# Performance work log

Hardware: AMD Instinct MI355X
Metric: run time of the kernel (lower is better)

The kernel has to match this reference:

```python
import jax, jax.numpy as jnp
import numpy as np

T, B, I, H, O = 512, 128, 512, 512, 12

def setup_inputs() -> dict:
    key = jax.random.key(0)
    ks = jax.random.split(key, 17)
    def w(k, shape):
        # xavier-normal-ish init
        std = float(np.sqrt(2.0 / (shape[0] + shape[-1])))
        return jax.random.normal(k, shape, dtype=jnp.float32) * std
    return {
        "x": jax.random.normal(ks[0], (T, B, I), dtype=jnp.float32),
        "w0": w(ks[1], (O, H)), "wz": w(ks[2], (O, H)), "wr": w(ks[3], (O, H)),
        "ws": w(ks[4], (I, H)),
        "wa": w(ks[5], (H, H)), "ua": w(ks[6], (I, H)), "va": w(ks[7], (H, 1)),
        "u0": w(ks[8], (H, H)), "uz": w(ks[9], (H, H)), "ur": w(ks[10], (H, H)),
        "c0": w(ks[11], (I, H)), "cz": w(ks[12], (I, H)), "cr": w(ks[13], (I, H)),
        "fc_w": w(ks[14], (H, O)),
        "fc_b": jnp.zeros((O,), dtype=jnp.float32),
        "max_labels": 16,
    }

def reference(x, w0, wz, wr, ws, wa, ua, va, u0, uz, ur, c0, cz, cr, fc_w, fc_b, max_labels):
    # x: [T, B, I] encoder states; decode max_labels steps of a Bahdanau-attention GRU.
    s0 = jnp.tanh(x[0] @ ws)              # [B, H]
    out0 = s0 @ fc_w + fc_b               # [B, O]
    U = jnp.einsum('tbi,ih->tbh', x, ua)  # precomputed encoder projection
    va_v = va[:, 0]                       # [H]

    def step(carry, _):
        s, out = carry                                          # [B,H], [B,O]
        e = jnp.einsum('tbh,h->tb', jnp.tanh(s @ wa + U), va_v)  # [T,B] additive scores
        a = jax.nn.softmax(e, axis=0)                           # attention over T
        c = jnp.einsum('tb,tbi->bi', a, x)                      # [B,I] context
        r = jax.nn.sigmoid(out @ wr + s @ ur + c @ cr)
        z = jax.nn.sigmoid(out @ wz + s @ uz + c @ cz)
        sh = jnp.tanh(out @ w0 + (r * s) @ u0 + c @ c0)
        s_new = (1.0 - z) * s + z * sh
        out_new = s_new @ fc_w + fc_b
        return (s_new, out_new), out_new

    _, outs = jax.lax.scan(step, (s0, out0), None, length=max_labels - 1)
    all_outs = jnp.concatenate([out0[None], outs], axis=0)  # [L, B, O]
    return jnp.transpose(all_outs, (1, 0, 2))               # [B, L, O]
```

## Files before the change

kernel.cpp:

```cpp
#include <hip/hip_runtime.h>

#define NSTEP 16

typedef __attribute__((ext_vector_type(8))) short s16x8;
typedef __attribute__((ext_vector_type(4))) float f32x4;
typedef __attribute__((ext_vector_type(2))) float f32x2;

__device__ __forceinline__ float bf2f(unsigned short u){
  union { unsigned int i; float f; } v; v.i = ((unsigned int)u) << 16; return v.f;
}
__device__ __forceinline__ unsigned short f2bf(float f){
  union { float f; unsigned int i; } v; v.f = f;
  unsigned int r = v.i + 0x7fffu + ((v.i >> 16) & 1u);
  return (unsigned short)(r >> 16);
}
__device__ __forceinline__ float fast_rcp(float x){ return __builtin_amdgcn_rcpf(x); }
__device__ __forceinline__ float fast_tanh(float x){
  float e = __expf(2.0f * x);
  return 1.0f - 2.0f * fast_rcp(e + 1.0f);
}
__device__ __forceinline__ float fast_sigmoid(float x){
  return fast_rcp(1.0f + __expf(-x));
}
__device__ __forceinline__ void gload16(const void* g, void* l){
  __builtin_amdgcn_global_load_lds((const __attribute__((address_space(1))) void*)g,
                                   (__attribute__((address_space(3))) void*)l, 16, 0, 0);
}
__device__ __forceinline__ float wave_sum(float v){
#pragma unroll
  for (int off = 32; off; off >>= 1) v += __shfl_xor(v, off, 64);
  return v;
}
__device__ __forceinline__ void fp8x8_dec(uint2 w, float* u){
  f32x2 d0 = __builtin_amdgcn_cvt_pk_f32_fp8(w.x, false);
  f32x2 d1 = __builtin_amdgcn_cvt_pk_f32_fp8(w.x, true);
  f32x2 d2 = __builtin_amdgcn_cvt_pk_f32_fp8(w.y, false);
  f32x2 d3 = __builtin_amdgcn_cvt_pk_f32_fp8(w.y, true);
  u[0] = d0[0]; u[1] = d0[1]; u[2] = d1[0]; u[3] = d1[1];
  u[4] = d2[0]; u[5] = d2[1]; u[6] = d3[0]; u[7] = d3[1];
}
__device__ __forceinline__ s16x8 f32x8_to_bf8(float4 a, float4 b){
  s16x8 t8;
  t8[0] = (short)f2bf(a.x); t8[1] = (short)f2bf(a.y);
  t8[2] = (short)f2bf(a.z); t8[3] = (short)f2bf(a.w);
  t8[4] = (short)f2bf(b.x); t8[5] = (short)f2bf(b.y);
  t8[6] = (short)f2bf(b.z); t8[7] = (short)f2bf(b.w);
  return t8;
}
__device__ __forceinline__ uint2 f32x8_to_fp8(float4 a, float4 b){
  unsigned int lo, hi;
  lo = __builtin_amdgcn_cvt_pk_fp8_f32(a.x, a.y, 0, false);
  lo = __builtin_amdgcn_cvt_pk_fp8_f32(a.z, a.w, lo, true);
  hi = __builtin_amdgcn_cvt_pk_fp8_f32(b.x, b.y, 0, false);
  hi = __builtin_amdgcn_cvt_pk_fp8_f32(b.z, b.w, hi, true);
  uint2 w; w.x = lo; w.y = hi;
  return w;
}
__device__ __forceinline__ unsigned char f2fp8(float f){
  return (unsigned char)(__builtin_amdgcn_cvt_pk_fp8_f32(f, f, 0, false) & 0xff);
}

struct GemmLDS { unsigned short A[128 * 64]; unsigned short B[128 * 64]; };

__global__ __launch_bounds__(512) void uxc_k(
    const float* __restrict__ x, const unsigned short* __restrict__ Bt,
    unsigned char* __restrict__ U8, unsigned char* __restrict__ x8){
  __shared__ GemmLDS lds;
  const int tid = threadIdx.x;
  const int lane = tid & 63, wid = tid >> 6;
  const int wr = wid >> 2, wc = wid & 3;
  const int mt = blockIdx.y, nt = blockIdx.x;
  f32x4 acc[4][2];
#pragma unroll
  for (int m = 0; m < 4; ++m)
#pragma unroll
    for (int n = 0; n < 2; ++n) acc[m][n] = (f32x4)0.0f;

  for (int kt = 0; kt < 512; kt += 64){
    __syncthreads();
    {
      bool emit = (kt >> 7) == nt;
#pragma unroll
      for (int i = 0; i < 2; ++i){
        int s = i * 512 + tid;
        int row = s >> 3, c8 = s & 7;
        int sc = c8 ^ (row & 7);
        size_t goff = (size_t)(mt * 128 + row) * 512 + kt + sc * 8;
        const float* ap = x + goff;
        float4 a0 = *(const float4*)ap, a1 = *(const float4*)(ap + 4);
        *(s16x8*)&lds.A[s * 8] = f32x8_to_bf8(a0, a1);
        if (emit) *(uint2*)(x8 + goff) = f32x8_to_fp8(a0, a1);
      }
#pragma unroll
      for (int p = 0; p < 2; ++p){
        int s = p * 512 + tid;
        int br = s >> 3, bkc = (s & 7) ^ (br & 7);
        gload16(Bt + (size_t)(nt * 128 + br) * 512 + kt + bkc * 8, &lds.B[s * 8]);
      }
    }
    __syncthreads();
#pragma unroll
    for (int ks = 0; ks < 2; ++ks){
      int kc_l = (lane >> 4) + ks * 4;
      s16x8 av[4], bv[2];
#pragma unroll
      for (int m = 0; m < 4; ++m){
        int r = wr * 64 + m * 16 + (lane & 15);
        av[m] = *(const s16x8*)&lds.A[r * 64 + ((kc_l ^ (r & 7)) << 3)];
      }
#pragma unroll
      for (int n = 0; n < 2; ++n){
        int c = wc * 32 + n * 16 + (lane & 15);
        bv[n] = *(const s16x8*)&lds.B[c * 64 + ((kc_l ^ (c & 7)) << 3)];
      }
#pragma unroll
      for (int m = 0; m < 4; ++m)
#pragma unroll
        for (int n = 0; n < 2; ++n)
          acc[m][n] = __builtin_amdgcn_mfma_f32_16x16x32_bf16(av[m], bv[n], acc[m][n], 0, 0, 0);
    }
  }
#pragma unroll
  for (int m = 0; m < 4; ++m)
#pragma unroll
    for (int n = 0; n < 2; ++n){
      int r_base = mt * 128 + wr * 64 + m * 16 + ((lane >> 4) << 2);
      int col = nt * 128 + wc * 32 + n * 16 + (lane & 15);
#pragma unroll
      for (int q = 0; q < 4; ++q)
        U8[(size_t)(r_base + q) * 512 + col] = f2fp8(acc[m][n][q]);
    }
}

struct FLDS { unsigned short A[64 * 256]; unsigned short B[64 * 256]; };

template<int EPI, bool AF32>
__device__ __forceinline__ void fgemm_body(int mt, int nt,
    const unsigned short* __restrict__ A, const float* __restrict__ Af,
    const unsigned short* __restrict__ Bt,
    unsigned short* __restrict__ ob0, float* __restrict__ o0,
    const float* __restrict__ e0, const float* __restrict__ e1,
    const float* __restrict__ e2, FLDS& lds){
  const int tid = threadIdx.x;
  const int lane = tid & 63, wid = tid >> 6;
  const int wr = wid >> 1, wc = wid & 1;
  f32x4 acc[2];
  acc[0] = (f32x4)0.0f; acc[1] = (f32x4)0.0f;

  for (int kt = 0; kt < 512; kt += 256){
    if (kt) __syncthreads();
#pragma unroll
    for (int i = 0; i < 4; ++i){
      int s = i * 512 + tid;
      int row = s >> 5, c = s & 31;
      int sc = (c & 24) | ((c & 7) ^ (row & 7));
      if constexpr (AF32){
        const float* ap = Af + (size_t)(mt * 64 + row) * 512 + kt + sc * 8;
        float4 a0 = *(const float4*)ap, a1 = *(const float4*)(ap + 4);
        *(s16x8*)&lds.A[s * 8] = f32x8_to_bf8(a0, a1);
      } else {
        gload16(A + (size_t)(mt * 64 + row) * 512 + kt + sc * 8, &lds.A[s * 8]);
      }
      gload16(Bt + (size_t)(nt * 64 + row) * 512 + kt + sc * 8, &lds.B[s * 8]);
    }
    __syncthreads();
#pragma unroll
    for (int kk = 0; kk < 8; ++kk){
      int kch = kk * 4 + (lane >> 4);
      int ar = wr * 16 + (lane & 15);
      int asw = (kch & 24) | ((kch & 7) ^ (ar & 7));
      s16x8 av = *(const s16x8*)&lds.A[ar * 256 + asw * 8];
#pragma unroll
      for (int n = 0; n < 2; ++n){
        int br = wc * 32 + n * 16 + (lane & 15);
        int bsw = (kch & 24) | ((kch & 7) ^ (br & 7));
        s16x8 bv = *(const s16x8*)&lds.B[br * 256 + bsw * 8];
        acc[n] = __builtin_amdgcn_mfma_f32_16x16x32_bf16(av, bv, acc[n], 0, 0, 0);
      }
    }
  }

#pragma unroll
  for (int n = 0; n < 2; ++n){
    int r_base = mt * 64 + wr * 16 + ((lane >> 4) << 2);
    int col = nt * 64 + wc * 32 + n * 16 + (lane & 15);
#pragma unroll
    for (int q = 0; q < 4; ++q){
      float v = acc[n][q];
      size_t r_ = (size_t)(r_base + q);
      if constexpr (EPI == 1){
        float t = fast_tanh(v);
        o0[r_ * 512 + col] = t;
        ob0[r_ * 512 + col] = f2bf(t);
      } else if constexpr (EPI == 2){
        o0[r_ * 2048 + col] = v + e0[col];
      } else if constexpr (EPI == 4){
        float v2 = v + e0[r_ * 512 + col];
        float sh = fast_tanh(v2);
        float z  = e1[r_ * 512 + col];
        float so = e2[r_ * 512 + col];
        float sn = (1.0f - z) * so + z * sh;
        o0[r_ * 512 + col] = sn;
        ob0[r_ * 512 + col] = f2bf(sn);
      }
    }
  }
}

template<int EPI, bool AF32>
__global__ __launch_bounds__(512) void fgemm_k(
    const unsigned short* __restrict__ A, const float* __restrict__ Af,
    const unsigned short* __restrict__ Bt,
    unsigned short* __restrict__ ob0, float* __restrict__ o0,
    const float* __restrict__ e0, const float* __restrict__ e1,
    const float* __restrict__ e2){
  __shared__ FLDS lds;
  fgemm_body<EPI, AF32>(blockIdx.y, blockIdx.x, A, Af, Bt, ob0, o0, e0, e1, e2, lds);
}

__global__ __launch_bounds__(512) void ec_k(const unsigned char* __restrict__ U8,
    const unsigned char* __restrict__ x8, const float* __restrict__ pre1,
    const float* __restrict__ va, float* __restrict__ cpart, float* __restrict__ psum){
  __shared__ float cred[8][512];
  __shared__ float pred[8];
  int chunk = blockIdx.x, b = blockIdx.y;
  int tid = threadIdx.x, lane = tid & 63, wid = tid >> 6;
  const float* pp = pre1 + (size_t)b * 2048 + lane * 8;
  float4 p0 = *(const float4*)pp, p1 = *(const float4*)(pp + 4);
  const float* vp = va + lane * 8;
  float4 v0 = *(const float4*)vp, v1 = *(const float4*)(vp + 4);
  float sv[8] = {p0.x, p0.y, p0.z, p0.w, p1.x, p1.y, p1.z, p1.w};
  float vv[8] = {v0.x, v0.y, v0.z, v0.w, v1.x, v1.y, v1.z, v1.w};
  float acc[8] = {0, 0, 0, 0, 0, 0, 0, 0};
  float psum_l = 0.f;
  int t0 = chunk * 256 + wid * 32;
  for (int i = 0; i < 32; ++i){
    int t = t0 + i;
    uint2 w = *(const uint2*)(U8 + ((size_t)t * 128 + b) * 512 + lane * 8);
    float u[8];
    fp8x8_dec(w, u);
    float e = 0.f;
#pragma unroll
    for (int k = 0; k < 8; ++k)
      e += fast_tanh(u[k] + sv[k]) * vv[k];
    e = wave_sum(e);
    float p = __expf(e);
    psum_l += p;
    uint2 wx = *(const uint2*)(x8 + ((size_t)t * 128 + b) * 512 + lane * 8);
    float ux[8];
    fp8x8_dec(wx, ux);
#pragma unroll
    for (int k = 0; k < 8; ++k) acc[k] += p * ux[k];
  }
#pragma unroll
  for (int k = 0; k < 8; ++k) cred[wid][lane * 8 + k] = acc[k];
  if (lane == 0) pred[wid] = psum_l;
  __syncthreads();
  float cs = 0.f;
#pragma unroll
  for (int w = 0; w < 8; ++w) cs += cred[w][tid];
  cpart[((size_t)chunk * 128 + b) * 512 + tid] = cs;
  if (tid == 0){
    float s = 0.f;
#pragma unroll
    for (int w = 0; w < 8; ++w) s += pred[w];
    psum[chunk * 128 + b] = s;
  }
}

__global__ __launch_bounds__(512) void gates_k(
    const float* __restrict__ cpart, const float* __restrict__ psum,
    const unsigned short* __restrict__ P2w, const float* __restrict__ pre1,
    const float* __restrict__ s_prev,
    unsigned short* __restrict__ rsb, float* __restrict__ zbuf, float* __restrict__ cu0){
  __shared__ FLDS lds;
  __shared__ float rden_s[64];
  const int tid = threadIdx.x;
  const int lane = tid & 63, wid = tid >> 6;
  const int wr = wid >> 1, wc = wid & 1;
  const int nt = blockIdx.x, mt = blockIdx.y;
  if (tid < 64){
    float d = psum[mt * 64 + tid] + psum[128 + mt * 64 + tid];
    rden_s[tid] = fast_rcp(d);
  }
  f32x4 acc[2];
  acc[0] = (f32x4)0.0f; acc[1] = (f32x4)0.0f;

  for (int kt = 0; kt < 512; kt += 256){
    __syncthreads();
#pragma unroll
    for (int i = 0; i < 4; ++i){
      int s = i * 512 + tid;
      int row = s >> 5, c = s & 31;
      int sc = (c & 24) | ((c & 7) ^ (row & 7));
      int b = mt * 64 + row;
      const float* cp0 = cpart + (size_t)b * 512 + kt + sc * 8;
      const float* cp1 = cp0 + (size_t)128 * 512;
      float rd = rden_s[row];
      float4 a0 = *(const float4*)cp0, a1 = *(const float4*)(cp0 + 4);
      float4 b0 = *(const float4*)cp1, b1 = *(const float4*)(cp1 + 4);
      s16x8 t8;
      t8[0] = (short)f2bf((a0.x + b0.x) * rd); t8[1] = (short)f2bf((a0.y + b0.y) * rd);
      t8[2] = (short)f2bf((a0.z + b0.z) * rd); t8[3] = (short)f2bf((a0.w + b0.w) * rd);
      t8[4] = (short)f2bf((a1.x + b1.x) * rd); t8[5] = (short)f2bf((a1.y + b1.y) * rd);
      t8[6] = (short)f2bf((a1.z + b1.z) * rd); t8[7] = (short)f2bf((a1.w + b1.w) * rd);
      *(s16x8*)&lds.A[s * 8] = t8;
      gload16(P2w + (size_t)(nt * 64 + row) * 512 + kt + sc * 8, &lds.B[s * 8]);
    }
    __syncthreads();
#pragma unroll
    for (int kk = 0; kk < 8; ++kk){
      int kch = kk * 4 + (lane >> 4);
      int ar = wr * 16 + (lane & 15);
      int asw = (kch & 24) | ((kch & 7) ^ (ar & 7));
      s16x8 av = *(const s16x8*)&lds.A[ar * 256 + asw * 8];
#pragma unroll
      for (int n = 0; n < 2; ++n){
        int br = wc * 32 + n * 16 + (lane & 15);
        int bsw = (kch & 24) | ((kch & 7) ^ (br & 7));
        s16x8 bv = *(const s16x8*)&lds.B[br * 256 + bsw * 8];
        acc[n] = __builtin_amdgcn_mfma_f32_16x16x32_bf16(av, bv, acc[n], 0, 0, 0);
      }
    }
  }

#pragma unroll
  for (int n = 0; n < 2; ++n){
    int r_base = mt * 64 + wr * 16 + ((lane >> 4) << 2);
    int col = nt * 64 + wc * 32 + n * 16 + (lane & 15);
#pragma unroll
    for (int q = 0; q < 4; ++q){
      float v = acc[n][q];
      size_t r_ = (size_t)(r_base + q);
      float v2 = v + pre1[r_ * 2048 + 512 + col];
      if (col < 512){
        float rg = fast_sigmoid(v2);
        rsb[r_ * 512 + col] = f2bf(rg * s_prev[r_ * 512 + col]);
      } else if (col < 1024){
        zbuf[r_ * 512 + (col - 512)] = fast_sigmoid(v2);
      } else {
        cu0[r_ * 512 + (col - 1024)] = v2;
      }
    }
  }
}

__global__ __launch_bounds__(512) void dout_k(const float* __restrict__ s_hist,
    const float* __restrict__ fcwT, const float* __restrict__ fcb,
    float* __restrict__ dout){
  int lane = threadIdx.x & 63, wid = threadIdx.x >> 6;
  int w = blockIdx.x * 8 + wid;
  int step = w >> 7, b = w & 127;
  const float* sp = s_hist + (size_t)w * 512 + lane * 8;
  float4 sa = *(const float4*)sp, sb = *(const float4*)(sp + 4);
#pragma unroll
  for (int o = 0; o < 12; ++o){
    const float* fp = fcwT + (size_t)o * 512 + lane * 8;
    float4 fa = *(const float4*)fp, fb = *(const float4*)(fp + 4);
    float sum = sa.x * fa.x + sa.y * fa.y + sa.z * fa.z + sa.w * fa.w +
                sb.x * fb.x + sb.y * fb.y + sb.z * fb.z + sb.w * fb.w;
    sum = wave_sum(sum);
    if (lane == 0)
      dout[(size_t)b * (NSTEP * 12) + step * 12 + o] = sum + fcb[o];
  }
}

__global__ __launch_bounds__(512) void trans_k(
    const float* __restrict__ ua, const float* __restrict__ wsm,
    const float* __restrict__ u0, const float* __restrict__ wa,
    const float* __restrict__ urm, const float* __restrict__ uz,
    const float* __restrict__ cr, const float* __restrict__ cz,
    const float* __restrict__ c0, const float* __restrict__ wrm,
    const float* __restrict__ wzm, const float* __restrict__ w0m,
    const float* __restrict__ fcw, const float* __restrict__ fcb,
    unsigned short* __restrict__ Pua, unsigned short* __restrict__ Pws,
    unsigned short* __restrict__ P3w, unsigned short* __restrict__ P1w,
    unsigned short* __restrict__ P2w, float* __restrict__ fcwT,
    float* __restrict__ bias_full){
  __shared__ unsigned short tr[64][72];
  int bid = blockIdx.x, tid = threadIdx.x;
  if (bid < 640){
    int mi = bid >> 6, tile = bid & 63;
    int trr = tile >> 3, tcc = tile & 7;
    const float* src = nullptr; const float* W = nullptr; unsigned short* dst;
    switch (mi){
      case 0: src = ua;  dst = Pua;               break;
      case 1: src = wsm; dst = Pws;               break;
      case 2: src = u0;  dst = P3w;               break;
      case 3: src = wa;  dst = P1w;               break;
      case 4: src = urm; dst = P1w + 512 * 512;  W = wrm; break;
      case 5: src = uz;  dst = P1w + 1024 * 512; W = wzm; break;
      case 6: src = nullptr; dst = P1w + 1536 * 512; W = w0m; break;
      case 7: src = cr;  dst = P2w;               break;
      case 8: src = cz;  dst = P2w + 512 * 512;   break;
      default:src = c0;  dst = P2w + 1024 * 512;  break;
    }
    int r = tid >> 3, c8 = (tid & 7) * 8;
    int h = trr * 64 + r;
    float vals[8];
    if (src){
      const float* sp = src + (size_t)h * 512 + tcc * 64 + c8;
      float4 a = *(const float4*)sp, b = *(const float4*)(sp + 4);
      vals[0] = a.x; vals[1] = a.y; vals[2] = a.z; vals[3] = a.w;
      vals[4] = b.x; vals[5] = b.y; vals[6] = b.z; vals[7] = b.w;
    } else {
#pragma unroll
      for (int k = 0; k < 8; ++k) vals[k] = 0.f;
    }
    if (W){
      float fr[12];
#pragma unroll
      for (int o = 0; o < 12; ++o) fr[o] = fcw[h * 12 + o];
#pragma unroll
      for (int jj = 0; jj < 8; ++jj){
        int j = tcc * 64 + c8 + jj;
        float cj = 0.f;
#pragma unroll
        for (int o = 0; o < 12; ++o) cj += fr[o] * W[o * 512 + j];
        vals[jj] += cj;
      }
    }
    unsigned short* lp = &tr[r][c8];
#pragma unroll
    for (int k = 0; k < 8; ++k) lp[k] = f2bf(vals[k]);
    __syncthreads();
    s16x8 o8v;
#pragma unroll
    for (int k = 0; k < 8; ++k) o8v[k] = (short)tr[c8 + k][r];
    *(s16x8*)(dst + (size_t)(tcc * 64 + r) * 512 + trr * 64 + c8) = o8v;
  } else if (bid < 652){
    int gidx = (bid - 640) * 512 + tid;
    int h = gidx / 12, o = gidx - h * 12;
    fcwT[(size_t)o * 512 + h] = fcw[h * 12 + o];
  } else {
#pragma unroll
    for (int p = 0; p < 4; ++p){
      int col = p * 512 + tid;
      float v = 0.f;
      if (p > 0){
        const float* W = (p == 1) ? wrm : (p == 2) ? wzm : w0m;
#pragma unroll
        for (int o = 0; o < 12; ++o) v += fcb[o] * W[o * 512 + tid];
      }
      bias_full[col] = v;
    }
  }
}

extern "C" void kernel_launch(void* const* d_in, const int* in_sizes, int n_in,
                              void* d_out, int out_size, void* d_ws, size_t ws_size,
                              hipStream_t stream){
  const float* x   = (const float*)d_in[0];
  const float* w0  = (const float*)d_in[1];
  const float* wz  = (const float*)d_in[2];
  const float* wrm = (const float*)d_in[3];
  const float* wsm = (const float*)d_in[4];
  const float* wa  = (const float*)d_in[5];
  const float* ua  = (const float*)d_in[6];
  const float* va  = (const float*)d_in[7];
  const float* u0  = (const float*)d_in[8];
  const float* uz  = (const float*)d_in[9];
  const float* urm = (const float*)d_in[10];
  const float* c0  = (const float*)d_in[11];
  const float* cz  = (const float*)d_in[12];
  const float* cr  = (const float*)d_in[13];
  const float* fcw = (const float*)d_in[14];
  const float* fcb = (const float*)d_in[15];
  float* dout = (float*)d_out;

  char* base = (char*)d_ws;
  size_t off = 0;
  auto alloc = [&](size_t bytes) -> char* {
    char* p = base + off; off += (bytes + 255) & ~(size_t)255; return p;
  };
  unsigned char*  x8   = (unsigned char*) alloc((size_t)512 * 128 * 512);
  unsigned char*  U8   = (unsigned char*) alloc((size_t)512 * 128 * 512);
  unsigned short* Pua  = (unsigned short*)alloc(512 * 512 * 2);
  unsigned short* Pws  = (unsigned short*)alloc(512 * 512 * 2);
  unsigned short* P3w  = (unsigned short*)alloc(512 * 512 * 2);
  unsigned short* P1w  = (unsigned short*)alloc((size_t)2048 * 512 * 2);
  unsigned short* P2w  = (unsigned short*)alloc((size_t)1536 * 512 * 2);
  float* fcwT          = (float*)alloc(12 * 512 * 4);
  float* bias_full     = (float*)alloc(2048 * 4);
  float* pre1          = (float*)alloc((size_t)128 * 2048 * 4);
  float* cpart         = (float*)alloc((size_t)2 * 128 * 512 * 4);
  float* psum          = (float*)alloc(2 * 128 * 4);
  unsigned short* rsb  = (unsigned short*)alloc((size_t)128 * 512 * 2);
  float* zbuf          = (float*)alloc((size_t)128 * 512 * 4);
  float* cu0           = (float*)alloc((size_t)128 * 512 * 4);
  float* s_hist        = (float*)alloc((size_t)NSTEP * 128 * 512 * 4);
  unsigned short* s_bf = (unsigned short*)alloc((size_t)128 * 512 * 2);
  (void)ws_size; (void)in_sizes; (void)n_in; (void)out_size;

  trans_k<<<653, 512, 0, stream>>>(ua, wsm, u0, wa, urm, uz, cr, cz, c0,
                                   wrm, wz, w0, fcw, fcb,
                                   Pua, Pws, P3w, P1w, P2w, fcwT, bias_full);
  uxc_k<<<dim3(4, 512), 512, 0, stream>>>(x, Pua, U8, x8);
  fgemm_k<1, true><<<dim3(8, 2), 512, 0, stream>>>(nullptr, x, Pws, s_bf, s_hist,
                                                   nullptr, nullptr, nullptr);

  for (int step = 1; step < NSTEP; ++step){
    const float* s_prev = s_hist + (size_t)(step - 1) * 128 * 512;
    float* s_cur = s_hist + (size_t)step * 128 * 512;
    fgemm_k<2, false><<<dim3(32, 2), 512, 0, stream>>>(s_bf, nullptr, P1w,
                                                       nullptr, pre1,
                                                       bias_full, nullptr, nullptr);
    ec_k<<<dim3(2, 128), 512, 0, stream>>>(U8, x8, pre1, va, cpart, psum);
    gates_k<<<dim3(24, 2), 512, 0, stream>>>(cpart, psum, P2w, pre1, s_prev,
                                             rsb, zbuf, cu0);
    fgemm_k<4, false><<<dim3(8, 2), 512, 0, stream>>>(rsb, nullptr, P3w,
                                                      s_bf, s_cur,
                                                      cu0, zbuf, s_prev);
  }
  dout_k<<<256, 512, 0, stream>>>(s_hist, fcwT, fcb, dout);
}
```

Measured before the change: 798.8 us.

## Split x cast into separate kernel and compute encoder projection with FP8 MFMA

The fused kernel that read fp32 x, converted it to bf16 for a bf16 MFMA GEMM and emitted fp8 x is replaced by two kernels. A standalone cast kernel writes x in fp8, and the U projection GEMM then loads fp8 x and an fp8 copy of ua (pre-scaled by 8, undone by 0.125) and uses fp8 MFMA. The aim is to stop each of the 4 column-tile blocks rereading fp32 x, and to halve LDS and operand bandwidth. In exchange it adds a kernel launch and uses a lower-precision fp8 weight operand, which costs accuracy.

```diff
diff --git a/kernel.cpp b/kernel.cpp
--- a/kernel.cpp
+++ b/kernel.cpp
@@ -60,12 +60,20 @@
   return (unsigned char)(__builtin_amdgcn_cvt_pk_fp8_f32(f, f, 0, false) & 0xff);
 }
 
-struct GemmLDS { unsigned short A[128 * 64]; unsigned short B[128 * 64]; };
-
-__global__ __launch_bounds__(512) void uxc_k(
-    const float* __restrict__ x, const unsigned short* __restrict__ Bt,
-    unsigned char* __restrict__ U8, unsigned char* __restrict__ x8){
-  __shared__ GemmLDS lds;
+__global__ __launch_bounds__(256) void castx_k(const float* __restrict__ x,
+                                               unsigned char* __restrict__ x8){
+  size_t idx = (size_t)blockIdx.x * 256 + threadIdx.x;
+  const float* p = x + idx * 8;
+  float4 a = *(const float4*)p, b = *(const float4*)(p + 4);
+  *(uint2*)(x8 + idx * 8) = f32x8_to_fp8(a, b);
+}
+
+struct G8LDS { unsigned char A[128 * 64]; unsigned char B[128 * 64]; };
+
+__global__ __launch_bounds__(512) void ugemm8_k(
+    const unsigned char* __restrict__ x8, const unsigned char* __restrict__ Pua8,
+    unsigned char* __restrict__ U8){
+  __shared__ G8LDS lds;
   const int tid = threadIdx.x;
   const int lane = tid & 63, wid = tid >> 6;
   const int wr = wid >> 2, wc = wid & 3;
@@ -76,48 +84,32 @@
 #pragma unroll
     for (int n = 0; n < 2; ++n) acc[m][n] = (f32x4)0.0f;
 
+  const int row = tid >> 2, j = tid & 3;
+  const int sc16 = j ^ (row & 3);
   for (int kt = 0; kt < 512; kt += 64){
     __syncthreads();
-    {
-      bool emit = (kt >> 7) == nt;
-#pragma unroll
-      for (int i = 0; i < 2; ++i){
-        int s = i * 512 + tid;
-        int row = s >> 3, c8 = s & 7;
-        int sc = c8 ^ (row & 7);
-        size_t goff = (size_t)(mt * 128 + row) * 512 + kt + sc * 8;
-        const float* ap = x + goff;
-        float4 a0 = *(const float4*)ap, a1 = *(const float4*)(ap + 4);
-        *(s16x8*)&lds.A[s * 8] = f32x8_to_bf8(a0, a1);
-        if (emit) *(uint2*)(x8 + goff) = f32x8_to_fp8(a0, a1);
-      }
-#pragma unroll
-      for (int p = 0; p < 2; ++p){
-        int s = p * 512 + tid;
-        int br = s >> 3, bkc = (s & 7) ^ (br & 7);
-        gload16(Bt + (size_t)(nt * 128 + br) * 512 + kt + bkc * 8, &lds.B[s * 8]);
-      }
-    }
+    gload16(x8  + (size_t)(mt * 128 + row) * 512 + kt + sc16 * 16, &lds.A[tid * 16]);
+    gload16(Pua8 + (size_t)(nt * 128 + row) * 512 + kt + sc16 * 16, &lds.B[tid * 16]);
     __syncthreads();
 #pragma unroll
     for (int ks = 0; ks < 2; ++ks){
-      int kc_l = (lane >> 4) + ks * 4;
-      s16x8 av[4], bv[2];
+      int g = (lane >> 4) + ks * 4;
+      long av[4], bv[2];
 #pragma unroll
       for (int m = 0; m < 4; ++m){
         int r = wr * 64 + m * 16 + (lane & 15);
-        av[m] = *(const s16x8*)&lds.A[r * 64 + ((kc_l ^ (r & 7)) << 3)];
+        av[m] = *(const long*)&lds.A[r * 64 + ((g ^ ((r & 3) << 1)) << 3)];
       }
 #pragma unroll
       for (int n = 0; n < 2; ++n){
         int c = wc * 32 + n * 16 + (lane & 15);
-        bv[n] = *(const s16x8*)&lds.B[c * 64 + ((kc_l ^ (c & 7)) << 3)];
+        bv[n] = *(const long*)&lds.B[c * 64 + ((g ^ ((c & 3) << 1)) << 3)];
       }
 #pragma unroll
       for (int m = 0; m < 4; ++m)
 #pragma unroll
         for (int n = 0; n < 2; ++n)
-          acc[m][n] = __builtin_amdgcn_mfma_f32_16x16x32_bf16(av[m], bv[n], acc[m][n], 0, 0, 0);
+          acc[m][n] = __builtin_amdgcn_mfma_f32_16x16x32_fp8_fp8(av[m], bv[n], acc[m][n], 0, 0, 0);
     }
   }
 #pragma unroll
@@ -128,7 +120,7 @@
       int col = nt * 128 + wc * 32 + n * 16 + (lane & 15);
 #pragma unroll
       for (int q = 0; q < 4; ++q)
-        U8[(size_t)(r_base + q) * 512 + col] = f2fp8(acc[m][n][q]);
+        U8[(size_t)(r_base + q) * 512 + col] = f2fp8(acc[m][n][q] * 0.125f);
     }
 }
 
@@ -373,7 +365,7 @@
     const float* __restrict__ c0, const float* __restrict__ wrm,
     const float* __restrict__ wzm, const float* __restrict__ w0m,
     const float* __restrict__ fcw, const float* __restrict__ fcb,
-    unsigned short* __restrict__ Pua, unsigned short* __restrict__ Pws,
+    unsigned char* __restrict__ Pua8, unsigned short* __restrict__ Pws,
     unsigned short* __restrict__ P3w, unsigned short* __restrict__ P1w,
     unsigned short* __restrict__ P2w, float* __restrict__ fcwT,
     float* __restrict__ bias_full){
@@ -382,9 +374,9 @@
   if (bid < 640){
     int mi = bid >> 6, tile = bid & 63;
     int trr = tile >> 3, tcc = tile & 7;
-    const float* src = nullptr; const float* W = nullptr; unsigned short* dst;
+    const float* src = nullptr; const float* W = nullptr; unsigned short* dst = nullptr;
     switch (mi){
-      case 0: src = ua;  dst = Pua;               break;
+      case 0: src = ua;  dst = nullptr;           break;
       case 1: src = wsm; dst = Pws;               break;
       case 2: src = u0;  dst = P3w;               break;
       case 3: src = wa;  dst = P1w;               break;
@@ -424,10 +416,19 @@
 #pragma unroll
     for (int k = 0; k < 8; ++k) lp[k] = f2bf(vals[k]);
     __syncthreads();
-    s16x8 o8v;
-#pragma unroll
-    for (int k = 0; k < 8; ++k) o8v[k] = (short)tr[c8 + k][r];
-    *(s16x8*)(dst + (size_t)(tcc * 64 + r) * 512 + trr * 64 + c8) = o8v;
+    if (mi == 0){
+      float v[8];
+#pragma unroll
+      for (int k = 0; k < 8; ++k) v[k] = bf2f(tr[c8 + k][r]) * 8.0f;
+      float4 a; a.x = v[0]; a.y = v[1]; a.z = v[2]; a.w = v[3];
+      float4 b; b.x = v[4]; b.y = v[5]; b.z = v[6]; b.w = v[7];
+      *(uint2*)(Pua8 + (size_t)(tcc * 64 + r) * 512 + trr * 64 + c8) = f32x8_to_fp8(a, b);
+    } else {
+      s16x8 o8v;
+#pragma unroll
+      for (int k = 0; k < 8; ++k) o8v[k] = (short)tr[c8 + k][r];
+      *(s16x8*)(dst + (size_t)(tcc * 64 + r) * 512 + trr * 64 + c8) = o8v;
+    }
   } else if (bid < 652){
     int gidx = (bid - 640) * 512 + tid;
     int h = gidx / 12, o = gidx - h * 12;
@@ -475,7 +476,7 @@
   };
   unsigned char*  x8   = (unsigned char*) alloc((size_t)512 * 128 * 512);
   unsigned char*  U8   = (unsigned char*) alloc((size_t)512 * 128 * 512);
-  unsigned short* Pua  = (unsigned short*)alloc(512 * 512 * 2);
+  unsigned char*  Pua8 = (unsigned char*) alloc(512 * 512);
   unsigned short* Pws  = (unsigned short*)alloc(512 * 512 * 2);
   unsigned short* P3w  = (unsigned short*)alloc(512 * 512 * 2);
   unsigned short* P1w  = (unsigned short*)alloc((size_t)2048 * 512 * 2);
@@ -494,8 +495,9 @@
 
   trans_k<<<653, 512, 0, stream>>>(ua, wsm, u0, wa, urm, uz, cr, cz, c0,
                                    wrm, wz, w0, fcw, fcb,
-                                   Pua, Pws, P3w, P1w, P2w, fcwT, bias_full);
-  uxc_k<<<dim3(4, 512), 512, 0, stream>>>(x, Pua, U8, x8);
+                                   Pua8, Pws, P3w, P1w, P2w, fcwT, bias_full);
+  castx_k<<<16384, 256, 0, stream>>>(x, x8);
+  ugemm8_k<<<dim3(4, 512), 512, 0, stream>>>(x8, Pua8, U8);
   fgemm_k<1, true><<<dim3(8, 2), 512, 0, stream>>>(nullptr, x, Pws, s_bf, s_hist,
                                                    nullptr, nullptr, nullptr);
 
```

Result: no change. 784.2 us (-1.8%).
